# Performance work log

Hardware: AMD Instinct MI355X
Metric: run time of the kernel (lower is better)

The kernel has to match this reference:

```python
import jax, jax.numpy as jnp
import numpy as np

D = 1024
N_A = 4096
N_V = 4096


def setup_inputs() -> dict:
    key = jax.random.key(0)
    ks = jax.random.split(key, 6)
    s = 1.0 / np.sqrt(D)  # like torch Linear default init scale
    return {
        "inputs_a": jax.random.normal(ks[0], (N_A, D), dtype=jnp.float32),
        "inputs_v": jax.random.normal(ks[1], (N_V, D), dtype=jnp.float32),
        "W_Ba": jax.random.uniform(ks[2], (D, D), jnp.float32, -s, s),
        "W_Aa": jax.random.uniform(ks[3], (D, D), jnp.float32, -s, s),
        "W_Bv": jax.random.uniform(ks[4], (D, D), jnp.float32, -s, s),
        "W_Av": jax.random.uniform(ks[5], (D, D), jnp.float32, -s, s),
    }


def reference(inputs_a, inputs_v, W_Ba, W_Aa, W_Bv, W_Av):
    # torch Linear: y = x @ W.T ; weights stored [out, in]
    a_a = inputs_a @ W_Aa.T                      # [N_a, D]
    b_a = inputs_a @ W_Ba.T                      # [N_a, D]
    a_v = inputs_v @ W_Av.T                      # [N_v, D]
    b_v = inputs_v @ W_Bv.T                      # [N_v, D]
    scores = b_a @ a_v.T                         # [N_a, N_v]
    alpha_av = jax.nn.softmax(scores, axis=1)    # softmax over N_v
    att_avv = alpha_av @ b_v                     # [N_a, D]
    att_vaa = alpha_av.T @ a_a                   # [N_v, D]
    feature_map_a = att_avv + inputs_a
    feature_map_v = att_vaa + inputs_v
    return feature_map_a, feature_map_v
```

## Files before the change

kernel.cpp:

```cpp
#include <hip/hip_runtime.h>
#include <stdint.h>

#define D_DIM 1024
#define NA_DIM 4096
#define NV_DIM 4096

typedef __bf16 bf16_t;
typedef __bf16 bf16x8 __attribute__((ext_vector_type(8)));
typedef float f32x4 __attribute__((ext_vector_type(4)));

__device__ __forceinline__ void gload_lds16(const void* g, void* lds) {
  __builtin_amdgcn_global_load_lds(
      (const __attribute__((address_space(1))) unsigned int*)g,
      (__attribute__((address_space(3))) unsigned int*)lds, 16, 0, 0);
}

#define VMW(N) asm volatile("s_waitcnt vmcnt(" #N ")" ::: "memory")

__device__ __forceinline__ void gemm256_8ph(const bf16_t* __restrict__ A,
                                            const bf16_t* __restrict__ B,
                                            int K, int kb, int klen, int bm, int bn,
                                            bf16_t* lds, f32x4 acc[8][4]) {
  const int tid = threadIdx.x;
  const int lane = tid & 63;
  const int wid = tid >> 6;
  const int wm = wid >> 2;
  const int wn = wid & 3;
  const int frow = lane & 15;
  const int hi = lane >> 4;
  const int k0e = ((hi ^ (frow & 7)) << 3);

  const int sr = (wid << 4) + (lane >> 3);
  const int sc = (((lane & 7) ^ (lane >> 3)) << 3);
  const bf16_t* pAs = A + (size_t)(bm + sr) * K + kb + sc;
  const bf16_t* pBs = B + (size_t)(bn + sr) * K + kb + sc;
  const int dstW = wid << 10;

  const int aBase = (wm << 13) + frow * 64 + k0e;
  const int bBase = 16384 + ((wn >> 1) << 13) + ((wn & 1) << 12) + frow * 64 + k0e;

#define STG_A(kt, h, bufb) do { \
    const bf16_t* s_ = pAs + (size_t)((h) * 128) * K + (size_t)(kt) * 64; \
    bf16_t* d_ = lds + (bufb) * 32768 + (h) * 8192 + dstW; \
    gload_lds16(s_, d_); gload_lds16(s_ + (size_t)8 * K, d_ + 512); } while (0)
#define STG_B(kt, h, bufb) do { \
    const bf16_t* s_ = pBs + (size_t)((h) * 128) * K + (size_t)(kt) * 64; \
    bf16_t* d_ = lds + (bufb) * 32768 + 16384 + (h) * 8192 + dstW; \
    gload_lds16(s_, d_); gload_lds16(s_ + (size_t)8 * K, d_ + 512); } while (0)

  bf16x8 bfr[4][2];

#define PHASE(BUFB, Q, ...) do { \
    asm volatile("s_barrier" ::: "memory"); \
    __VA_ARGS__; \
    const bf16_t* Lb = lds + (BUFB) * 32768; \
    if ((Q) == 0) { \
      _Pragma("unroll") for (int fc = 0; fc < 4; ++fc) { \
        bfr[fc][0] = *(const bf16x8*)&Lb[bBase + fc * 1024]; \
        bfr[fc][1] = *(const bf16x8*)&Lb[(bBase ^ 32) + fc * 1024]; \
      } \
    } \
    bf16x8 a00 = *(const bf16x8*)&Lb[aBase + (Q) * 2048]; \
    bf16x8 a01 = *(const bf16x8*)&Lb[(aBase ^ 32) + (Q) * 2048]; \
    bf16x8 a10 = *(const bf16x8*)&Lb[aBase + (Q) * 2048 + 1024]; \
    bf16x8 a11 = *(const bf16x8*)&Lb[(aBase ^ 32) + (Q) * 2048 + 1024]; \
    __builtin_amdgcn_s_setprio(1); \
    _Pragma("unroll") for (int fc = 0; fc < 4; ++fc) { \
      acc[(Q) * 2][fc]     = __builtin_amdgcn_mfma_f32_16x16x32_bf16(a00, bfr[fc][0], acc[(Q) * 2][fc], 0, 0, 0); \
      acc[(Q) * 2][fc]     = __builtin_amdgcn_mfma_f32_16x16x32_bf16(a01, bfr[fc][1], acc[(Q) * 2][fc], 0, 0, 0); \
      acc[(Q) * 2 + 1][fc] = __builtin_amdgcn_mfma_f32_16x16x32_bf16(a10, bfr[fc][0], acc[(Q) * 2 + 1][fc], 0, 0, 0); \
      acc[(Q) * 2 + 1][fc] = __builtin_amdgcn_mfma_f32_16x16x32_bf16(a11, bfr[fc][1], acc[(Q) * 2 + 1][fc], 0, 0, 0); \
    } \
    __builtin_amdgcn_s_setprio(0); \
    asm volatile("s_waitcnt lgkmcnt(0)" ::: "memory"); \
  } while (0)

  const int NI = klen >> 7;

  STG_B(0, 0, 0); STG_B(0, 1, 0); STG_A(0, 0, 0); STG_A(0, 1, 0);
  STG_B(1, 0, 1); STG_B(1, 1, 1);

  for (int it = 0; it < NI; ++it) {
    const int T = 2 * it;
    const bool more = (it + 1 < NI);
    VMW(4);
    PHASE(0, 0, { STG_A(T + 1, 0, 1); });
    PHASE(0, 1, { STG_A(T + 1, 1, 1); });
    PHASE(0, 2, { if (more) STG_B(T + 2, 0, 0); });
    PHASE(0, 3, { if (more) STG_B(T + 2, 1, 0); });
    if (more) { VMW(4); } else { VMW(0); }
    PHASE(1, 0, { if (more) STG_A(T + 2, 0, 0); });
    PHASE(1, 1, { if (more) STG_A(T + 2, 1, 0); });
    PHASE(1, 2, { if (more) STG_B(T + 3, 0, 1); });
    PHASE(1, 3, { if (more) STG_B(T + 3, 1, 1); });
  }
#undef PHASE
#undef STG_A
#undef STG_B
}

template <int BF16OUT>
__device__ __forceinline__ void store256(void* Cv, int ldc, int bm, int bn, f32x4 acc[8][4]) {
  const int lane = threadIdx.x & 63;
  const int wid = threadIdx.x >> 6;
  const int wm = wid >> 2, wn = wid & 3;
  const int frow = lane & 15, hi = lane >> 4;
  const int row0 = bm + wm * 128 + hi * 4;
  const int col0 = bn + wn * 64 + frow;
#pragma unroll
  for (int rf = 0; rf < 8; ++rf)
#pragma unroll
    for (int fc = 0; fc < 4; ++fc)
#pragma unroll
      for (int r = 0; r < 4; ++r) {
        size_t idx = (size_t)(row0 + rf * 16 + r) * ldc + (col0 + fc * 16);
        if constexpr (BF16OUT) ((bf16_t*)Cv)[idx] = (bf16_t)acc[rf][fc][r];
        else ((float*)Cv)[idx] = acc[rf][fc][r];
      }
}

__global__ __launch_bounds__(512, 2) void gemm_proj4(
    const bf16_t* __restrict__ Xa, const bf16_t* __restrict__ Xv,
    const bf16_t* __restrict__ W0, const bf16_t* __restrict__ W1,
    const bf16_t* __restrict__ W2, const bf16_t* __restrict__ W3,
    bf16_t* __restrict__ C0, bf16_t* __restrict__ C1,
    bf16_t* __restrict__ C2, bf16_t* __restrict__ C3) {
  __shared__ bf16_t lds[65536];
  const int z = blockIdx.z;
  const bf16_t* A = (z < 2) ? Xa : Xv;
  const bf16_t* B = (z == 0) ? W0 : (z == 1) ? W1 : (z == 2) ? W2 : W3;
  bf16_t* C = (z == 0) ? C0 : (z == 1) ? C1 : (z == 2) ? C2 : C3;
  f32x4 acc[8][4] = {};
  gemm256_8ph(A, B, D_DIM, 0, D_DIM, blockIdx.x * 256, blockIdx.y * 256, lds, acc);
  store256<1>(C, D_DIM, blockIdx.x * 256, blockIdx.y * 256, acc);
}

__global__ __launch_bounds__(512, 2) void gemm_scores(const bf16_t* __restrict__ A,
                                                      const bf16_t* __restrict__ B,
                                                      float* __restrict__ C) {
  __shared__ bf16_t lds[65536];
  f32x4 acc[8][4] = {};
  gemm256_8ph(A, B, D_DIM, 0, D_DIM, blockIdx.x * 256, blockIdx.y * 256, lds, acc);
  store256<0>(C, NV_DIM, blockIdx.x * 256, blockIdx.y * 256, acc);
}

__global__ __launch_bounds__(512, 2) void gemm_splitk(
    const bf16_t* __restrict__ alpha, const bf16_t* __restrict__ bvT,
    const bf16_t* __restrict__ alphaT, const bf16_t* __restrict__ aaT,
    float* __restrict__ P) {
  __shared__ bf16_t lds[65536];
  const int z = blockIdx.z;
  const bf16_t* A = (z < 2) ? alpha : alphaT;
  const bf16_t* B = (z < 2) ? bvT : aaT;
  const int kb = (z & 1) * 2048;
  f32x4 acc[8][4] = {};
  gemm256_8ph(A, B, 4096, kb, 2048, blockIdx.x * 256, blockIdx.y * 256, lds, acc);
  store256<0>(P + (size_t)z * NA_DIM * D_DIM, D_DIM, blockIdx.x * 256, blockIdx.y * 256, acc);
}

__global__ __launch_bounds__(256) void reduce_splitk(const float* __restrict__ P,
                                                     const float* __restrict__ resA,
                                                     const float* __restrict__ resV,
                                                     float* __restrict__ out) {
  const int g = blockIdx.y;
  const size_t n = (size_t)NA_DIM * D_DIM;
  size_t i = ((size_t)blockIdx.x * 256 + threadIdx.x) * 4;
  const float* p0 = P + (size_t)g * 2 * n;
  const float* p1 = p0 + n;
  const float* r = g ? resV : resA;
  float4 a = *(const float4*)(p0 + i);
  float4 b = *(const float4*)(p1 + i);
  float4 c = *(const float4*)(r + i);
  float4 o = {a.x + b.x + c.x, a.y + b.y + c.y, a.z + b.z + c.z, a.w + b.w + c.w};
  *(float4*)(out + g * n + i) = o;
}

__device__ __forceinline__ void cvt8(const float* in, bf16_t* out, int i) {
  float4 v0 = *(const float4*)(in + i);
  float4 v1 = *(const float4*)(in + i + 4);
  bf16x8 o;
  o[0] = (bf16_t)v0.x; o[1] = (bf16_t)v0.y; o[2] = (bf16_t)v0.z; o[3] = (bf16_t)v0.w;
  o[4] = (bf16_t)v1.x; o[5] = (bf16_t)v1.y; o[6] = (bf16_t)v1.z; o[7] = (bf16_t)v1.w;
  *(bf16x8*)(out + i) = o;
}

__global__ __launch_bounds__(256) void cvt2(const float* __restrict__ inA,
                                            const float* __restrict__ inV,
                                            bf16_t* __restrict__ oA,
                                            bf16_t* __restrict__ oV) {
  const float* in = blockIdx.y ? inV : inA;
  bf16_t* out = blockIdx.y ? oV : oA;
  cvt8(in, out, (blockIdx.x * 256 + threadIdx.x) * 8);
}

__global__ __launch_bounds__(256) void cvt4(const float* __restrict__ i0, const float* __restrict__ i1,
                                            const float* __restrict__ i2, const float* __restrict__ i3,
                                            bf16_t* __restrict__ o0, bf16_t* __restrict__ o1,
                                            bf16_t* __restrict__ o2, bf16_t* __restrict__ o3) {
  const int z = blockIdx.y;
  const float* in = (z == 0) ? i0 : (z == 1) ? i1 : (z == 2) ? i2 : i3;
  bf16_t* out = (z == 0) ? o0 : (z == 1) ? o1 : (z == 2) ? o2 : o3;
  cvt8(in, out, (blockIdx.x * 256 + threadIdx.x) * 8);
}

__global__ __launch_bounds__(256) void softmax_rows(const float* __restrict__ S,
                                                    bf16_t* __restrict__ P) {
  const int row = blockIdx.x;
  const int ncol = 4096;
  const float* s = S + (size_t)row * ncol;
  const int base = threadIdx.x * 16;
  float v[16];
  float4* vp = (float4*)v;
#pragma unroll
  for (int q = 0; q < 4; ++q) vp[q] = *(const float4*)(s + base + q * 4);
  float m = v[0];
#pragma unroll
  for (int q = 1; q < 16; ++q) m = fmaxf(m, v[q]);
  for (int off = 32; off; off >>= 1) m = fmaxf(m, __shfl_xor(m, off));
  __shared__ float sm[4], ss[4];
  const int wid = threadIdx.x >> 6, lane = threadIdx.x & 63;
  if (lane == 0) sm[wid] = m;
  __syncthreads();
  m = fmaxf(fmaxf(sm[0], sm[1]), fmaxf(sm[2], sm[3]));
  float sum = 0.f;
#pragma unroll
  for (int q = 0; q < 16; ++q) { v[q] = __expf(v[q] - m); sum += v[q]; }
  for (int off = 32; off; off >>= 1) sum += __shfl_xor(sum, off);
  if (lane == 0) ss[wid] = sum;
  __syncthreads();
  const float inv = 1.0f / (ss[0] + ss[1] + ss[2] + ss[3]);
  bf16x8 o0, o1;
#pragma unroll
  for (int q = 0; q < 8; ++q) { o0[q] = (bf16_t)(v[q] * inv); o1[q] = (bf16_t)(v[q + 8] * inv); }
  bf16_t* p = P + (size_t)row * ncol + base;
  *(bf16x8*)p = o0;
  *(bf16x8*)(p + 8) = o1;
}

__global__ __launch_bounds__(256) void transpose_bf16(const bf16_t* __restrict__ in,
                                                      bf16_t* __restrict__ out, int R, int C) {
  __shared__ bf16_t t[64][72];
  const int bx = blockIdx.x * 64;
  const int by = blockIdx.y * 64;
  const int tid = threadIdx.x;
  const int c8 = (tid & 7) * 8;
  const int r = tid >> 3;
#pragma unroll
  for (int rr = 0; rr < 64; rr += 32) {
    bf16x8 v = *(const bf16x8*)(in + (size_t)(by + r + rr) * C + bx + c8);
    *(bf16x8*)&t[r + rr][c8] = v;
  }
  __syncthreads();
#pragma unroll
  for (int rr = 0; rr < 64; rr += 32) {
    bf16x8 v;
#pragma unroll
    for (int q = 0; q < 8; ++q) v[q] = t[c8 + q][r + rr];
    *(bf16x8*)(out + (size_t)(bx + r + rr) * R + by + c8) = v;
  }
}

extern "C" void kernel_launch(void* const* d_in, const int* in_sizes, int n_in,
                              void* d_out, int out_size, void* d_ws, size_t ws_size,
                              hipStream_t stream) {
  (void)in_sizes; (void)n_in; (void)out_size; (void)ws_size;
  const float* inA = (const float*)d_in[0];
  const float* inV = (const float*)d_in[1];
  const float* wBa = (const float*)d_in[2];
  const float* wAa = (const float*)d_in[3];
  const float* wBv = (const float*)d_in[4];
  const float* wAv = (const float*)d_in[5];
  float* out = (float*)d_out;

  char* w = (char*)d_ws;
  auto take = [&](size_t bytes) { void* p = (void*)w; w += bytes; return p; };
  const size_t XB = (size_t)NA_DIM * D_DIM * 2;
  const size_t WB = (size_t)D_DIM * D_DIM * 2;
  bf16_t* XaB = (bf16_t*)take(XB);
  bf16_t* XvB = (bf16_t*)take(XB);
  bf16_t* WBaB = (bf16_t*)take(WB);
  bf16_t* WAaB = (bf16_t*)take(WB);
  bf16_t* WBvB = (bf16_t*)take(WB);
  bf16_t* WAvB = (bf16_t*)take(WB);
  bf16_t* b_a = (bf16_t*)take(XB);
  bf16_t* a_v = (bf16_t*)take(XB);
  bf16_t* a_a = (bf16_t*)take(XB);
  bf16_t* b_v = (bf16_t*)take(XB);
  bf16_t* a_aT = (bf16_t*)take(XB);
  bf16_t* b_vT = (bf16_t*)take(XB);
  float* scores = (float*)take((size_t)NA_DIM * NV_DIM * 4);
  bf16_t* alpha = (bf16_t*)take((size_t)NA_DIM * NV_DIM * 2);
  bf16_t* alphaT = (bf16_t*)take((size_t)NA_DIM * NV_DIM * 2);
  float* P = scores;

  cvt2<<<dim3(NA_DIM * D_DIM / 2048, 2), 256, 0, stream>>>(inA, inV, XaB, XvB);
  cvt4<<<dim3(D_DIM * D_DIM / 2048, 4), 256, 0, stream>>>(wBa, wAa, wAv, wBv,
                                                          WBaB, WAaB, WAvB, WBvB);

  gemm_proj4<<<dim3(NA_DIM / 256, D_DIM / 256, 4), 512, 0, stream>>>(
      XaB, XvB, WBaB, WAaB, WAvB, WBvB, b_a, a_a, a_v, b_v);

  gemm_scores<<<dim3(NA_DIM / 256, NV_DIM / 256), 512, 0, stream>>>(b_a, a_v, scores);

  softmax_rows<<<NA_DIM, 256, 0, stream>>>(scores, alpha);

  transpose_bf16<<<dim3(NV_DIM / 64, NA_DIM / 64), 256, 0, stream>>>(alpha, alphaT, NA_DIM, NV_DIM);
  transpose_bf16<<<dim3(D_DIM / 64, NA_DIM / 64), 256, 0, stream>>>(a_a, a_aT, NA_DIM, D_DIM);
  transpose_bf16<<<dim3(D_DIM / 64, NV_DIM / 64), 256, 0, stream>>>(b_v, b_vT, NV_DIM, D_DIM);

  gemm_splitk<<<dim3(NA_DIM / 256, D_DIM / 256, 4), 512, 0, stream>>>(
      alpha, b_vT, alphaT, a_aT, P);
  reduce_splitk<<<dim3(NA_DIM * D_DIM / 1024, 2), 256, 0, stream>>>(P, inA, inV, out);
}
```

Measured before the change: 208.4 us.

## Software-pipeline LDS fragment reads one phase ahead of MFMA compute

Restructures the 8-phase GEMM main loop so LDS reads of the A/B fragments for the next phase are issued before the MFMAs of the current phase. Double-buffered register fragments, partial lgkmcnt waits and sched_barriers replace the read-then-wait-then-compute pattern. This is meant to hide LDS latency behind matrix-core work. It costs more VGPRs for the extra fragment buffers and relies on exact waitcnt counts being correct.

Measured after the change: 224.6 us. 7.8% more time.

```diff
diff --git a/kernel.cpp b/kernel.cpp
--- a/kernel.cpp
+++ b/kernel.cpp
@@ -16,6 +16,9 @@
 }
 
 #define VMW(N) asm volatile("s_waitcnt vmcnt(" #N ")" ::: "memory")
+#define LKW(N) asm volatile("s_waitcnt lgkmcnt(" #N ")" ::: "memory")
+#define SB0() __builtin_amdgcn_sched_barrier(0)
+#define BAR() asm volatile("s_barrier" ::: "memory")
 
 __device__ __forceinline__ void gemm256_8ph(const bf16_t* __restrict__ A,
                                             const bf16_t* __restrict__ B,
@@ -48,53 +51,56 @@
     bf16_t* d_ = lds + (bufb) * 32768 + 16384 + (h) * 8192 + dstW; \
     gload_lds16(s_, d_); gload_lds16(s_ + (size_t)8 * K, d_ + 512); } while (0)
 
-  bf16x8 bfr[4][2];
-
-#define PHASE(BUFB, Q, ...) do { \
-    asm volatile("s_barrier" ::: "memory"); \
-    __VA_ARGS__; \
-    const bf16_t* Lb = lds + (BUFB) * 32768; \
-    if ((Q) == 0) { \
-      _Pragma("unroll") for (int fc = 0; fc < 4; ++fc) { \
-        bfr[fc][0] = *(const bf16x8*)&Lb[bBase + fc * 1024]; \
-        bfr[fc][1] = *(const bf16x8*)&Lb[(bBase ^ 32) + fc * 1024]; \
-      } \
-    } \
-    bf16x8 a00 = *(const bf16x8*)&Lb[aBase + (Q) * 2048]; \
-    bf16x8 a01 = *(const bf16x8*)&Lb[(aBase ^ 32) + (Q) * 2048]; \
-    bf16x8 a10 = *(const bf16x8*)&Lb[aBase + (Q) * 2048 + 1024]; \
-    bf16x8 a11 = *(const bf16x8*)&Lb[(aBase ^ 32) + (Q) * 2048 + 1024]; \
+  bf16x8 aF[2][4];
+  bf16x8 bF[2][4][2];
+
+#define READ_A(S, BUFB, Q) do { const bf16_t* Lb_ = lds + (BUFB) * 32768; \
+    aF[S][0] = *(const bf16x8*)&Lb_[aBase + (Q) * 2048]; \
+    aF[S][1] = *(const bf16x8*)&Lb_[(aBase ^ 32) + (Q) * 2048]; \
+    aF[S][2] = *(const bf16x8*)&Lb_[aBase + (Q) * 2048 + 1024]; \
+    aF[S][3] = *(const bf16x8*)&Lb_[(aBase ^ 32) + (Q) * 2048 + 1024]; } while (0)
+#define READ_B(S, BUFB) do { const bf16_t* Lb_ = lds + (BUFB) * 32768; \
+    _Pragma("unroll") for (int fc = 0; fc < 4; ++fc) { \
+      bF[S][fc][0] = *(const bf16x8*)&Lb_[bBase + fc * 1024]; \
+      bF[S][fc][1] = *(const bf16x8*)&Lb_[(bBase ^ 32) + fc * 1024]; } } while (0)
+
+#define MFMA16(AS, BS, Q) do { \
     __builtin_amdgcn_s_setprio(1); \
     _Pragma("unroll") for (int fc = 0; fc < 4; ++fc) { \
-      acc[(Q) * 2][fc]     = __builtin_amdgcn_mfma_f32_16x16x32_bf16(a00, bfr[fc][0], acc[(Q) * 2][fc], 0, 0, 0); \
-      acc[(Q) * 2][fc]     = __builtin_amdgcn_mfma_f32_16x16x32_bf16(a01, bfr[fc][1], acc[(Q) * 2][fc], 0, 0, 0); \
-      acc[(Q) * 2 + 1][fc] = __builtin_amdgcn_mfma_f32_16x16x32_bf16(a10, bfr[fc][0], acc[(Q) * 2 + 1][fc], 0, 0, 0); \
-      acc[(Q) * 2 + 1][fc] = __builtin_amdgcn_mfma_f32_16x16x32_bf16(a11, bfr[fc][1], acc[(Q) * 2 + 1][fc], 0, 0, 0); \
+      acc[(Q) * 2][fc]     = __builtin_amdgcn_mfma_f32_16x16x32_bf16(aF[AS][0], bF[BS][fc][0], acc[(Q) * 2][fc], 0, 0, 0); \
+      acc[(Q) * 2][fc]     = __builtin_amdgcn_mfma_f32_16x16x32_bf16(aF[AS][1], bF[BS][fc][1], acc[(Q) * 2][fc], 0, 0, 0); \
+      acc[(Q) * 2 + 1][fc] = __builtin_amdgcn_mfma_f32_16x16x32_bf16(aF[AS][2], bF[BS][fc][0], acc[(Q) * 2 + 1][fc], 0, 0, 0); \
+      acc[(Q) * 2 + 1][fc] = __builtin_amdgcn_mfma_f32_16x16x32_bf16(aF[AS][3], bF[BS][fc][1], acc[(Q) * 2 + 1][fc], 0, 0, 0); \
     } \
-    __builtin_amdgcn_s_setprio(0); \
-    asm volatile("s_waitcnt lgkmcnt(0)" ::: "memory"); \
-  } while (0)
+    __builtin_amdgcn_s_setprio(0); } while (0)
 
   const int NI = klen >> 7;
 
   STG_B(0, 0, 0); STG_B(0, 1, 0); STG_A(0, 0, 0); STG_A(0, 1, 0);
   STG_B(1, 0, 1); STG_B(1, 1, 1);
+  VMW(4);
+  BAR();
+  READ_B(0, 0); READ_A(0, 0, 0);
 
   for (int it = 0; it < NI; ++it) {
     const int T = 2 * it;
     const bool more = (it + 1 < NI);
-    VMW(4);
-    PHASE(0, 0, { STG_A(T + 1, 0, 1); });
-    PHASE(0, 1, { STG_A(T + 1, 1, 1); });
-    PHASE(0, 2, { if (more) STG_B(T + 2, 0, 0); });
-    PHASE(0, 3, { if (more) STG_B(T + 2, 1, 0); });
-    if (more) { VMW(4); } else { VMW(0); }
-    PHASE(1, 0, { if (more) STG_A(T + 2, 0, 0); });
-    PHASE(1, 1, { if (more) STG_A(T + 2, 1, 0); });
-    PHASE(1, 2, { if (more) STG_B(T + 3, 0, 1); });
-    PHASE(1, 3, { if (more) STG_B(T + 3, 1, 1); });
+    BAR(); STG_A(T + 1, 0, 1); READ_A(1, 0, 1); LKW(4); SB0(); MFMA16(0, 0, 0);
+    BAR(); STG_A(T + 1, 1, 1); READ_A(0, 0, 2); LKW(4); SB0(); MFMA16(1, 0, 1);
+    BAR(); if (more) STG_B(T + 2, 0, 0); READ_A(1, 0, 3); LKW(4); SB0(); MFMA16(0, 0, 2);
+    BAR(); if (more) { STG_B(T + 2, 1, 0); VMW(4); } else { VMW(0); }
+    READ_B(1, 1); READ_A(0, 1, 0); LKW(12); SB0(); MFMA16(1, 0, 3);
+    BAR(); if (more) STG_A(T + 2, 0, 0); READ_A(1, 1, 1); LKW(4); SB0(); MFMA16(0, 1, 0);
+    BAR(); if (more) STG_A(T + 2, 1, 0); READ_A(0, 1, 2); LKW(4); SB0(); MFMA16(1, 1, 1);
+    BAR(); if (more) STG_B(T + 3, 0, 1); READ_A(1, 1, 3); LKW(4); SB0(); MFMA16(0, 1, 2);
+    BAR();
+    if (more) { STG_B(T + 3, 1, 1); VMW(4); READ_B(0, 0); READ_A(0, 0, 0); LKW(12); }
+    else { LKW(0); }
+    SB0(); MFMA16(1, 1, 3);
   }
-#undef PHASE
+#undef MFMA16
+#undef READ_A
+#undef READ_B
 #undef STG_A
 #undef STG_B
 }
```
